# Kernel optimization log

Measured on AMD Instinct MI355X. Metric: run time of the kernel, lower is better.

Reference implementation:

```python
import jax, jax.numpy as jnp
import numpy as np

B, L, D = 8, 1024, 1024  # L must equal D for the elementwise sqrt(K) divide to broadcast


def setup_inputs() -> dict:
    key = jax.random.key(0)
    ks = jax.random.split(key, 9)
    # Non-negative inputs/weights/biases so K = x @ Wk.T + bk >= 0 and sqrt(K) is finite.
    rc = jax.random.uniform(ks[0], (B, L, D), dtype=jnp.float32)
    ri = jax.random.uniform(ks[1], (B, L, D), dtype=jnp.float32)
    tc = jax.random.uniform(ks[2], (B, L, D), dtype=jnp.float32)
    scale = 0.02
    Wq = jax.random.uniform(ks[3], (D, D), dtype=jnp.float32) * scale
    Wk = jax.random.uniform(ks[4], (D, D), dtype=jnp.float32) * scale
    Wv = jax.random.uniform(ks[5], (D, D), dtype=jnp.float32) * scale
    bq = jax.random.uniform(ks[6], (D,), dtype=jnp.float32) * scale
    bk = jax.random.uniform(ks[7], (D,), dtype=jnp.float32) * scale
    bv = jax.random.uniform(ks[8], (D,), dtype=jnp.float32) * scale
    return {
        "reference_caption": rc,
        "reference_image": ri,
        "target_caption": tc,
        "Wq": Wq, "bq": bq,
        "Wk": Wk, "bk": bk,
        "Wv": Wv, "bv": bv,
    }


def reference(reference_caption, reference_image, target_caption, Wq, bq, Wk, bk, Wv, bv):
    # torch nn.Linear: y = x @ W.T + b
    Q = reference_caption @ Wq.T + bq          # [B, Lq, D]
    K = reference_image @ Wk.T + bk            # [B, Lk, D]
    V = reference_image @ Wv.T + bv            # [B, Lk, D]
    matmul_qk = jnp.einsum("bqd,bkd->bqk", Q, K)  # [B, Lq, Lk]
    # Faithful to source: elementwise divide by sqrt(K) tensor (broadcasts since Lq==Lk==D).
    scaled_logits = matmul_qk / jnp.sqrt(K)
    attention_weights = jax.nn.softmax(scaled_logits, axis=-1)
    output = jnp.einsum("bqk,bkd->bqd", attention_weights, V)
    return (output, attention_weights)
```

## Files before the change

kernel.cpp:

```cpp
#include <hip/hip_runtime.h>
#include <hip/hip_fp16.h>
#include <math.h>

typedef unsigned short u16;
typedef __attribute__((ext_vector_type(8))) _Float16 half8;
typedef __attribute__((ext_vector_type(4))) float f32x4;

#define ASLOT 4096
#define SLOT  12288

__device__ __forceinline__ u16 f2h(float f){ __half h=__float2half(f); u16 r; __builtin_memcpy(&r,&h,2); return r; }
__device__ __forceinline__ float h2f(u16 u){ __half h; __builtin_memcpy(&h,&u,2); return __half2float(h); }

template<int ROWS>
__device__ __forceinline__ void stage_tile(const u16* __restrict__ G, int rowbase, int ldg,
                                           int k0, u16* Ls, int tid){
#pragma unroll
    for (int p = 0; p < ROWS / 64; ++p){
        const int lin = tid + p * 256;
        const int row = lin >> 2;
        const int cg  = ((lin & 3) ^ ((row >> 1) & 3)) * 8;
        const u16* g = G + (size_t)(rowbase + row) * ldg + (k0 + cg);
        __builtin_amdgcn_global_load_lds(
            (__attribute__((address_space(1))) void*)g,
            (__attribute__((address_space(3))) void*)(Ls + (size_t)lin * 8), 16, 0, 0);
    }
}

template<int EPI, int BIASM>
__device__ __forceinline__ void gemm_core(
    const u16* __restrict__ A, const u16* __restrict__ B,
    const float* __restrict__ bias,
    float* __restrict__ of, u16* __restrict__ oh,
    const float* __restrict__ cm, u16* __restrict__ od,
    int by, int bx, int lda, int ldb, int ldc, int K, u16* sh)
{
    const int tid  = threadIdx.x;
    const int lane = tid & 63, wv = tid >> 6;
    const int wr = (wv >> 1) * 64;
    const int wc = (wv & 1) * 128;
    const int row0 = by * 128, col0 = bx * 256;
    const int lr = lane & 15, hi = lane >> 4;
    const int co = (hi ^ ((lr >> 1) & 3)) * 8;

    f32x4 acc[4][8];
#pragma unroll
    for (int m = 0; m < 4; m++)
#pragma unroll
        for (int n = 0; n < 8; n++) acc[m][n] = (f32x4){0.f, 0.f, 0.f, 0.f};

    auto stage_set = [&](int buf, int k0){
        u16* s = sh + buf * SLOT;
        stage_tile<128>(A, row0, lda, k0, s, tid);
        stage_tile<256>(B, col0, ldb, k0, s + ASLOT, tid);
    };

    const int NIT = K >> 5;
    stage_set(0, 0);
    stage_set(1, 32);
    int bufs = 2, bufr = 0;
    for (int t = 0; t < NIT; ++t){
        if (t + 2 < NIT){ stage_set(bufs, (t + 2) << 5); bufs = (bufs + 1 == 3) ? 0 : bufs + 1; }
        const int rem = NIT - 1 - t;
        if (rem >= 2)      asm volatile("s_waitcnt vmcnt(12)" ::: "memory");
        else if (rem == 1) asm volatile("s_waitcnt vmcnt(6)" ::: "memory");
        else               asm volatile("s_waitcnt vmcnt(0)" ::: "memory");
        __builtin_amdgcn_s_barrier();
        __builtin_amdgcn_sched_barrier(0);

        const u16* s = sh + bufr * SLOT;
        bufr = (bufr + 1 == 3) ? 0 : bufr + 1;

        half8 a[4], b[8];
#pragma unroll
        for (int m = 0; m < 4; m++) a[m] = *(const half8*)&s[(wr + m * 16 + lr) * 32 + co];
#pragma unroll
        for (int n = 0; n < 8; n++) b[n] = *(const half8*)&s[ASLOT + (wc + n * 16 + lr) * 32 + co];
#pragma unroll
        for (int m = 0; m < 4; m++)
#pragma unroll
            for (int n = 0; n < 8; n++)
                acc[m][n] = __builtin_amdgcn_mfma_f32_16x16x32_f16(a[m], b[n], acc[m][n], 0, 0, 0);
        __builtin_amdgcn_sched_barrier(0);
        __builtin_amdgcn_s_barrier();
    }

#pragma unroll
    for (int m = 0; m < 4; m++) {
        const int rb = row0 + wr + m * 16 + hi * 4;
#pragma unroll
        for (int n = 0; n < 8; n++) {
            const int c = col0 + wc + n * 16 + lr;
            const float bc = (BIASM == 1) ? bias[c] : 0.f;
#pragma unroll
            for (int q = 0; q < 4; q++) {
                const int r = rb + q;
                float v = acc[m][n][q] + bc;
                if (BIASM == 2) v += bias[r];
                const size_t idx = (size_t)r * ldc + c;
                if (EPI == 0) of[idx] = v;
                else if (EPI == 1) oh[idx] = f2h(v);
                else {
                    const float d  = v - cm[(size_t)((r >> 10) << 10) + c];
                    const u16  dh = f2h(d);
                    oh[idx] = dh;
                    od[idx] = f2h(d - h2f(dh));
                }
            }
        }
    }
}

__global__ __launch_bounds__(256, 2) void lin_qk_k(
    const u16* __restrict__ rc_h, const u16* __restrict__ ri_h,
    const u16* __restrict__ Wq_h, const u16* __restrict__ Wk_h,
    const float* __restrict__ bq, const float* __restrict__ bk,
    const float* __restrict__ cm,
    u16* __restrict__ Q_h, u16* __restrict__ Kd, u16* __restrict__ Krs)
{
    __shared__ __align__(16) u16 sh[3 * SLOT];
    const int nwg = gridDim.x, chunk = nwg >> 3;
    const int swz = ((int)blockIdx.x & 7) * chunk + ((int)blockIdx.x >> 3);
    const int p = swz & 1, t = swz >> 1;
    if (p == 0) {
        gemm_core<1, 1>(rc_h, Wq_h, bq, nullptr, Q_h, nullptr, nullptr,
                        t >> 2, t & 3, 1024, 1024, 1024, 1024, sh);
    } else {
        gemm_core<5, 1>(ri_h, Wk_h, bk, nullptr, Kd, cm, Krs,
                        t >> 2, t & 3, 1024, 1024, 1024, 1024, sh);
    }
}

__global__ __launch_bounds__(256, 2) void qkt_vt_k(
    const u16* __restrict__ Q_h, const u16* __restrict__ Kd,
    const u16* __restrict__ ri_h, const u16* __restrict__ Wv_h,
    const float* __restrict__ bv, const float* __restrict__ u,
    float* __restrict__ wts, u16* __restrict__ Vt)
{
    __shared__ __align__(16) u16 sh[3 * SLOT];
    const int nwg = gridDim.x, chunk = nwg >> 3;
    const int swz = ((int)blockIdx.x & 7) * chunk + ((int)blockIdx.x >> 3);
    const int p = swz & 1, t = swz >> 1;
    if (p == 0) {
        const int z = t >> 5, rem = t & 31;
        gemm_core<0, 2>(Q_h + ((size_t)z << 20), Kd + ((size_t)z << 20),
                        u + ((size_t)z << 10), wts + ((size_t)z << 20), nullptr,
                        nullptr, nullptr,
                        rem >> 2, rem & 3, 1024, 1024, 1024, 1024, sh);
    } else {
        gemm_core<1, 2>(Wv_h, ri_h, bv, nullptr, Vt, nullptr, nullptr,
                        t >> 5, t & 31, 1024, 1024, 8192, 1024, sh);
    }
}

__global__ __launch_bounds__(256, 2) void av_k(
    const u16* __restrict__ W_h, const u16* __restrict__ Vt, float* __restrict__ outp)
{
    __shared__ __align__(16) u16 sh[3 * SLOT];
    const int nwg = gridDim.x, chunk = nwg >> 3;
    const int wg = ((int)blockIdx.x & 7) * chunk + ((int)blockIdx.x >> 3);
    const int z = wg >> 5, rem = wg & 31;
    gemm_core<0, 0>(W_h + ((size_t)z << 20), Vt + (size_t)z * 1024,
                    nullptr, outp + ((size_t)z << 20), nullptr, nullptr, nullptr,
                    rem >> 2, rem & 3, 1024, 8192, 1024, 1024, sh);
}

__global__ __launch_bounds__(256)
void colmean_k(const u16* __restrict__ ri_h, float* __restrict__ xbar)
{
    const int b = blockIdx.x >> 5, sub = blockIdx.x & 31;
    const int dg = sub & 3, rg = sub >> 2;
    const int d = dg * 256 + threadIdx.x;
    const u16* base = ri_h + ((size_t)b << 20) + ((size_t)(rg * 128) << 10) + d;
    float s = 0.f;
#pragma unroll 4
    for (int r = 0; r < 128; ++r) s += h2f(base[(size_t)r << 10]);
    atomicAdd(&xbar[(b << 10) + d], s * (1.f / 1024.f));
}

template<bool BIAS, bool AFULL>
__global__ __launch_bounds__(256)
void rowdot_k(const u16* __restrict__ A, const float* __restrict__ B,
              const float* __restrict__ bias, float* __restrict__ out)
{
    const int o = blockIdx.x * 4 + (threadIdx.x >> 6);
    const int lane = threadIdx.x & 63;
    const int ar = AFULL ? o : (o & 1023);
    const int br = o >> 10;
    const u16* ap = A + ((size_t)ar << 10);
    const float* bp = B + ((size_t)br << 10);
    float s = 0.f;
#pragma unroll
    for (int j = 0; j < 16; ++j){ const int i = lane + (j << 6); s += h2f(ap[i]) * bp[i]; }
#pragma unroll
    for (int off = 32; off >= 1; off >>= 1) s += __shfl_xor(s, off);
    if (lane == 0) out[o] = s + (BIAS ? bias[ar] : 0.f);
}

__global__ __launch_bounds__(256)
void softmax_scale_k(float* __restrict__ W, const u16* __restrict__ Kd,
                     const u16* __restrict__ Krs, const float* __restrict__ cm,
                     u16* __restrict__ Wh)
{
    const long row = blockIdx.x;
    const int b = (int)(row >> 10);
    float* p = W + (row << 10);
    const int tid = threadIdx.x;

    float4 v = ((const float4*)p)[tid];
    const ushort4 kd = ((const ushort4*)(Kd + (row << 10)))[tid];
    const ushort4 ks = ((const ushort4*)(Krs + (row << 10)))[tid];
    const float4 cmv = ((const float4*)(cm + ((size_t)b << 10)))[tid];
    v.x *= rsqrtf(h2f(kd.x) + h2f(ks.x) + cmv.x);
    v.y *= rsqrtf(h2f(kd.y) + h2f(ks.y) + cmv.y);
    v.z *= rsqrtf(h2f(kd.z) + h2f(ks.z) + cmv.z);
    v.w *= rsqrtf(h2f(kd.w) + h2f(ks.w) + cmv.w);

    float m = fmaxf(fmaxf(v.x, v.y), fmaxf(v.z, v.w));
#pragma unroll
    for (int o = 32; o >= 1; o >>= 1) m = fmaxf(m, __shfl_xor(m, o));
    __shared__ float sm[4];
    const int wid = tid >> 6, lane = tid & 63;
    if (lane == 0) sm[wid] = m;
    __syncthreads();
    m = fmaxf(fmaxf(sm[0], sm[1]), fmaxf(sm[2], sm[3]));

    v.x = __expf(v.x - m); v.y = __expf(v.y - m);
    v.z = __expf(v.z - m); v.w = __expf(v.w - m);
    float s = v.x + v.y + v.z + v.w;
#pragma unroll
    for (int o = 32; o >= 1; o >>= 1) s += __shfl_xor(s, o);
    __shared__ float ss[4];
    if (lane == 0) ss[wid] = s;
    __syncthreads();
    s = ss[0] + ss[1] + ss[2] + ss[3];

    const float inv = 1.0f / s;
    v.x *= inv; v.y *= inv; v.z *= inv; v.w *= inv;
    ((float4*)p)[tid] = v;

    ushort4 ub;
    ub.x = f2h(v.x); ub.y = f2h(v.y); ub.z = f2h(v.z); ub.w = f2h(v.w);
    ((ushort4*)(Wh + (row << 10)))[tid] = ub;
}

__global__ __launch_bounds__(256)
void conv_plain5_k(const float4* __restrict__ x0, ushort4* __restrict__ y0,
                   const float4* __restrict__ x1, ushort4* __restrict__ y1,
                   const float4* __restrict__ x2, ushort4* __restrict__ y2,
                   const float4* __restrict__ x3, ushort4* __restrict__ y3,
                   const float4* __restrict__ x4, ushort4* __restrict__ y4)
{
    const long i = (long)blockIdx.x * 256 + threadIdx.x;
    const long n0 = 2097152, n1 = 262144;
    const float4* x; ushort4* y; long j;
    if (i < n0)                 { x = x0; y = y0; j = i; }
    else if (i < 2*n0)          { x = x1; y = y1; j = i - n0; }
    else if (i < 2*n0 + n1)     { x = x2; y = y2; j = i - 2*n0; }
    else if (i < 2*n0 + 2*n1)   { x = x3; y = y3; j = i - 2*n0 - n1; }
    else                        { x = x4; y = y4; j = i - 2*n0 - 2*n1; }
    const float4 v = x[j];
    ushort4 o;
    o.x = f2h(v.x); o.y = f2h(v.y); o.z = f2h(v.z); o.w = f2h(v.w);
    y[j] = o;
}

extern "C" void kernel_launch(void* const* d_in, const int* in_sizes, int n_in,
                              void* d_out, int out_size, void* d_ws, size_t ws_size,
                              hipStream_t stream)
{
    const float* rc = (const float*)d_in[0];
    const float* ri = (const float*)d_in[1];
    const float* Wq = (const float*)d_in[3];
    const float* bq = (const float*)d_in[4];
    const float* Wk = (const float*)d_in[5];
    const float* bk = (const float*)d_in[6];
    const float* Wv = (const float*)d_in[7];
    const float* bv = (const float*)d_in[8];

    const long M8 = 8192 * 1024L;
    const long M1 = 1024 * 1024L;

    u16* ws   = (u16*)d_ws;
    u16* ri_h = ws;
    u16* rc_h = ws + 1 * M8;
    u16* Kd   = ws + 2 * M8;
    u16* Krs  = ws + 3 * M8;
    u16* Wq_h = ws + 4 * M8;
    u16* Wk_h = Wq_h + M1;
    u16* Wv_h = Wk_h + M1;
    float* xbar = (float*)(ws + 4 * M8 + 3 * M1);
    float* cm   = xbar + 8192;
    float* uu   = cm + 8192;

    float* outp = (float*)d_out;
    float* wts  = outp + M8;
    u16*   Q_h  = (u16*)d_out;
    u16*   Vt   = rc_h;
    u16*   W_h  = ri_h;

    conv_plain5_k<<<19456, 256, 0, stream>>>(
        (const float4*)ri, (ushort4*)ri_h, (const float4*)rc, (ushort4*)rc_h,
        (const float4*)Wq, (ushort4*)Wq_h, (const float4*)Wk, (ushort4*)Wk_h,
        (const float4*)Wv, (ushort4*)Wv_h);

    hipMemsetAsync(xbar, 0, 8192 * sizeof(float), stream);
    colmean_k<<<256, 256, 0, stream>>>(ri_h, xbar);

    rowdot_k<true, false><<<2048, 256, 0, stream>>>(Wk_h, xbar, bk, cm);

    lin_qk_k<<<512, 256, 0, stream>>>(rc_h, ri_h, Wq_h, Wk_h, bq, bk, cm, Q_h, Kd, Krs);

    rowdot_k<false, true><<<2048, 256, 0, stream>>>(Q_h, cm, nullptr, uu);

    qkt_vt_k<<<512, 256, 0, stream>>>(Q_h, Kd, ri_h, Wv_h, bv, uu, wts, Vt);

    softmax_scale_k<<<8192, 256, 0, stream>>>(wts, Kd, Krs, cm, W_h);

    av_k<<<256, 256, 0, stream>>>(W_h, Vt, outp);
}
```

Measured before the change: 166.4 us.

## Use 256x256 tiles with 8-wave ping-pong pipelined GEMM for projection kernels

Replaces the 128x256, 4-wave, triple-buffered GEMM core with a 256x256-tile, 512-thread, double-buffered core for the Q/K projection and QK^T/V^T kernels. The new core uses K-steps of 64, an 8-column XOR swizzle, and interleaves staging loads with MFMA phases using barriers and s_setprio. The aim is higher arithmetic intensity per tile and better overlap of loads with MFMA. In exchange it launches half as many workgroups at one block per CU, which could leave CUs underused, and it needs 128KB of LDS. The AV kernel keeps the old core under a new name.

```diff
diff --git a/kernel.cpp b/kernel.cpp
--- a/kernel.cpp
+++ b/kernel.cpp
@@ -12,23 +12,14 @@
 __device__ __forceinline__ u16 f2h(float f){ __half h=__float2half(f); u16 r; __builtin_memcpy(&r,&h,2); return r; }
 __device__ __forceinline__ float h2f(u16 u){ __half h; __builtin_memcpy(&h,&u,2); return __half2float(h); }
 
-template<int ROWS>
-__device__ __forceinline__ void stage_tile(const u16* __restrict__ G, int rowbase, int ldg,
-                                           int k0, u16* Ls, int tid){
-#pragma unroll
-    for (int p = 0; p < ROWS / 64; ++p){
-        const int lin = tid + p * 256;
-        const int row = lin >> 2;
-        const int cg  = ((lin & 3) ^ ((row >> 1) & 3)) * 8;
-        const u16* g = G + (size_t)(rowbase + row) * ldg + (k0 + cg);
-        __builtin_amdgcn_global_load_lds(
-            (__attribute__((address_space(1))) void*)g,
-            (__attribute__((address_space(3))) void*)(Ls + (size_t)lin * 8), 16, 0, 0);
-    }
-}
+#define SYNC1 do{ __builtin_amdgcn_sched_barrier(0); __builtin_amdgcn_s_barrier(); \
+    asm volatile("s_waitcnt lgkmcnt(0)" ::: "memory"); __builtin_amdgcn_sched_barrier(0); \
+    __builtin_amdgcn_s_setprio(1); }while(0)
+#define SYNC2 do{ __builtin_amdgcn_s_setprio(0); __builtin_amdgcn_sched_barrier(0); \
+    __builtin_amdgcn_s_barrier(); }while(0)
 
 template<int EPI, int BIASM>
-__device__ __forceinline__ void gemm_core(
+__device__ __forceinline__ void gemm8(
     const u16* __restrict__ A, const u16* __restrict__ B,
     const float* __restrict__ bias,
     float* __restrict__ of, u16* __restrict__ oh,
@@ -37,63 +28,111 @@
 {
     const int tid  = threadIdx.x;
     const int lane = tid & 63, wv = tid >> 6;
-    const int wr = (wv >> 1) * 64;
-    const int wc = (wv & 1) * 128;
-    const int row0 = by * 128, col0 = bx * 256;
+    const int wr = (wv >> 2) * 128;
+    const int wc = (wv & 3) * 64;
+    const int row0 = by * 256, col0 = bx * 256;
     const int lr = lane & 15, hi = lane >> 4;
-    const int co = (hi ^ ((lr >> 1) & 3)) * 8;
-
-    f32x4 acc[4][8];
-#pragma unroll
-    for (int m = 0; m < 4; m++)
-#pragma unroll
-        for (int n = 0; n < 8; n++) acc[m][n] = (f32x4){0.f, 0.f, 0.f, 0.f};
-
-    auto stage_set = [&](int buf, int k0){
-        u16* s = sh + buf * SLOT;
-        stage_tile<128>(A, row0, lda, k0, s, tid);
-        stage_tile<256>(B, col0, ldb, k0, s + ASLOT, tid);
+
+    f32x4 acc[8][4];
+#pragma unroll
+    for (int m = 0; m < 8; m++)
+#pragma unroll
+        for (int n = 0; n < 4; n++) acc[m][n] = (f32x4){0.f, 0.f, 0.f, 0.f};
+
+    auto STG = [&](int op, int kt, int half){
+        const u16* G = op ? B : A;
+        const int  ld = op ? ldb : lda;
+        const int  rb = (op ? col0 : row0) + half * 128;
+        const int  k0 = kt << 6;
+        u16* dst = sh + ((kt & 1) << 15) + (op << 14) + (half << 13);
+#pragma unroll
+        for (int p = 0; p < 2; ++p){
+            const int lin = tid + p * 512;
+            const int r   = lin >> 3;
+            const int cg  = (lin & 7) ^ (r & 7);
+            const u16* g = G + (size_t)(rb + r) * ld + k0 + cg * 8;
+            __builtin_amdgcn_global_load_lds(
+                (__attribute__((address_space(1))) void*)g,
+                (__attribute__((address_space(3))) void*)(dst + (size_t)lin * 8), 16, 0, 0);
+        }
     };
-
-    const int NIT = K >> 5;
-    stage_set(0, 0);
-    stage_set(1, 32);
-    int bufs = 2, bufr = 0;
-    for (int t = 0; t < NIT; ++t){
-        if (t + 2 < NIT){ stage_set(bufs, (t + 2) << 5); bufs = (bufs + 1 == 3) ? 0 : bufs + 1; }
-        const int rem = NIT - 1 - t;
-        if (rem >= 2)      asm volatile("s_waitcnt vmcnt(12)" ::: "memory");
-        else if (rem == 1) asm volatile("s_waitcnt vmcnt(6)" ::: "memory");
-        else               asm volatile("s_waitcnt vmcnt(0)" ::: "memory");
-        __builtin_amdgcn_s_barrier();
-        __builtin_amdgcn_sched_barrier(0);
-
-        const u16* s = sh + bufr * SLOT;
-        bufr = (bufr + 1 == 3) ? 0 : bufr + 1;
-
-        half8 a[4], b[8];
-#pragma unroll
-        for (int m = 0; m < 4; m++) a[m] = *(const half8*)&s[(wr + m * 16 + lr) * 32 + co];
-#pragma unroll
-        for (int n = 0; n < 8; n++) b[n] = *(const half8*)&s[ASLOT + (wc + n * 16 + lr) * 32 + co];
-#pragma unroll
-        for (int m = 0; m < 4; m++)
-#pragma unroll
-            for (int n = 0; n < 8; n++)
-                acc[m][n] = __builtin_amdgcn_mfma_f32_16x16x32_f16(a[m], b[n], acc[m][n], 0, 0, 0);
-        __builtin_amdgcn_sched_barrier(0);
-        __builtin_amdgcn_s_barrier();
-    }
-
-#pragma unroll
-    for (int m = 0; m < 4; m++) {
+    auto LDA_ = [&](half8* a, int kt, int mh){
+        const u16* base = sh + ((kt & 1) << 15) + ((wr >> 7) << 13);
+#pragma unroll
+        for (int mi = 0; mi < 4; ++mi)
+#pragma unroll
+            for (int ks = 0; ks < 2; ++ks){
+                const int row = (mh * 4 + mi) * 16 + lr;
+                a[mi * 2 + ks] = *(const half8*)&base[row * 64 + (((hi + ks * 4) ^ (lr & 7)) * 8)];
+            }
+    };
+    auto LDB_ = [&](half8* b, int kt, int nh){
+        const u16* base = sh + ((kt & 1) << 15) + 16384 + ((wc >> 7) << 13);
+        const int wcl = wc & 127;
+#pragma unroll
+        for (int ni = 0; ni < 2; ++ni)
+#pragma unroll
+            for (int ks = 0; ks < 2; ++ks){
+                const int row = wcl + (nh * 2 + ni) * 16 + lr;
+                b[ni * 2 + ks] = *(const half8*)&base[row * 64 + (((hi + ks * 4) ^ (lr & 7)) * 8)];
+            }
+    };
+    auto MM = [&](half8* a, half8* b, int mh, int nh){
+#pragma unroll
+        for (int mi = 0; mi < 4; ++mi)
+#pragma unroll
+            for (int ni = 0; ni < 2; ++ni)
+#pragma unroll
+                for (int ks = 0; ks < 2; ++ks)
+                    acc[mh * 4 + mi][nh * 2 + ni] = __builtin_amdgcn_mfma_f32_16x16x32_f16(
+                        a[mi * 2 + ks], b[ni * 2 + ks], acc[mh * 4 + mi][nh * 2 + ni], 0, 0, 0);
+    };
+
+    const int NKT = K >> 6, NIT = NKT >> 1;
+    STG(0, 0, 0); STG(0, 0, 1); STG(1, 0, 0); STG(1, 0, 1);
+    STG(1, 1, 0); STG(1, 1, 1); STG(0, 1, 0);
+    asm volatile("s_waitcnt vmcnt(6)" ::: "memory");
+    __builtin_amdgcn_s_barrier();
+
+    half8 a[8], b0[4], b1[4];
+    for (int i = 0; i < NIT; ++i){
+        const int t0 = 2 * i, t1 = 2 * i + 1;
+        const bool m0 = (t0 + 2 < NKT), m1 = (t1 + 2 < NKT);
+        LDA_(a, t0, 0); LDB_(b0, t0, 0);
+        STG(0, t1, 1);
+        SYNC1; MM(a, b0, 0, 0); SYNC2;
+        LDB_(b1, t0, 1);
+        SYNC1; MM(a, b1, 0, 1); SYNC2;
+        LDA_(a, t0, 1);
+        if (m0) STG(1, t0 + 2, 0);
+        SYNC1; MM(a, b1, 1, 1); SYNC2;
+        if (m0) { STG(1, t0 + 2, 1); STG(0, t0 + 2, 0); }
+        if (m0) asm volatile("s_waitcnt vmcnt(6)" ::: "memory");
+        else    asm volatile("s_waitcnt vmcnt(0)" ::: "memory");
+        SYNC1; MM(a, b0, 1, 0); SYNC2;
+        LDA_(a, t1, 0); LDB_(b0, t1, 0);
+        if (m0) STG(0, t0 + 2, 1);
+        SYNC1; MM(a, b0, 0, 0); SYNC2;
+        LDB_(b1, t1, 1);
+        SYNC1; MM(a, b1, 0, 1); SYNC2;
+        LDA_(a, t1, 1);
+        if (m1) STG(1, t1 + 2, 0);
+        SYNC1; MM(a, b1, 1, 1); SYNC2;
+        if (m1) { STG(1, t1 + 2, 1); STG(0, t1 + 2, 0); }
+        if (m1) asm volatile("s_waitcnt vmcnt(6)" ::: "memory");
+        else    asm volatile("s_waitcnt vmcnt(0)" ::: "memory");
+        SYNC1; MM(a, b0, 1, 0); SYNC2;
+    }
+
+#pragma unroll
+    for (int m = 0; m < 8; m++){
         const int rb = row0 + wr + m * 16 + hi * 4;
 #pragma unroll
-        for (int n = 0; n < 8; n++) {
+        for (int n = 0; n < 4; n++){
             const int c = col0 + wc + n * 16 + lr;
             const float bc = (BIASM == 1) ? bias[c] : 0.f;
 #pragma unroll
-            for (int q = 0; q < 4; q++) {
+            for (int q = 0; q < 4; q++){
                 const int r = rb + q;
                 float v = acc[m][n][q] + bc;
                 if (BIASM == 2) v += bias[r];
@@ -111,45 +150,126 @@
     }
 }
 
-__global__ __launch_bounds__(256, 2) void lin_qk_k(
+__global__ __launch_bounds__(512, 1) void lin_qk_k(
     const u16* __restrict__ rc_h, const u16* __restrict__ ri_h,
     const u16* __restrict__ Wq_h, const u16* __restrict__ Wk_h,
     const float* __restrict__ bq, const float* __restrict__ bk,
     const float* __restrict__ cm,
     u16* __restrict__ Q_h, u16* __restrict__ Kd, u16* __restrict__ Krs)
 {
-    __shared__ __align__(16) u16 sh[3 * SLOT];
+    __shared__ __align__(16) u16 sh[65536];
     const int nwg = gridDim.x, chunk = nwg >> 3;
     const int swz = ((int)blockIdx.x & 7) * chunk + ((int)blockIdx.x >> 3);
     const int p = swz & 1, t = swz >> 1;
     if (p == 0) {
-        gemm_core<1, 1>(rc_h, Wq_h, bq, nullptr, Q_h, nullptr, nullptr,
-                        t >> 2, t & 3, 1024, 1024, 1024, 1024, sh);
+        gemm8<1, 1>(rc_h, Wq_h, bq, nullptr, Q_h, nullptr, nullptr,
+                    t >> 2, t & 3, 1024, 1024, 1024, 1024, sh);
     } else {
-        gemm_core<5, 1>(ri_h, Wk_h, bk, nullptr, Kd, cm, Krs,
-                        t >> 2, t & 3, 1024, 1024, 1024, 1024, sh);
-    }
-}
-
-__global__ __launch_bounds__(256, 2) void qkt_vt_k(
+        gemm8<5, 1>(ri_h, Wk_h, bk, nullptr, Kd, cm, Krs,
+                    t >> 2, t & 3, 1024, 1024, 1024, 1024, sh);
+    }
+}
+
+__global__ __launch_bounds__(512, 1) void qkt_vt_k(
     const u16* __restrict__ Q_h, const u16* __restrict__ Kd,
     const u16* __restrict__ ri_h, const u16* __restrict__ Wv_h,
     const float* __restrict__ bv, const float* __restrict__ u,
     float* __restrict__ wts, u16* __restrict__ Vt)
 {
-    __shared__ __align__(16) u16 sh[3 * SLOT];
+    __shared__ __align__(16) u16 sh[65536];
     const int nwg = gridDim.x, chunk = nwg >> 3;
     const int swz = ((int)blockIdx.x & 7) * chunk + ((int)blockIdx.x >> 3);
     const int p = swz & 1, t = swz >> 1;
     if (p == 0) {
-        const int z = t >> 5, rem = t & 31;
-        gemm_core<0, 2>(Q_h + ((size_t)z << 20), Kd + ((size_t)z << 20),
-                        u + ((size_t)z << 10), wts + ((size_t)z << 20), nullptr,
-                        nullptr, nullptr,
-                        rem >> 2, rem & 3, 1024, 1024, 1024, 1024, sh);
+        const int z = t >> 4, rem = t & 15;
+        gemm8<0, 2>(Q_h + ((size_t)z << 20), Kd + ((size_t)z << 20),
+                    u + ((size_t)z << 10), wts + ((size_t)z << 20), nullptr,
+                    nullptr, nullptr,
+                    rem >> 2, rem & 3, 1024, 1024, 1024, 1024, sh);
     } else {
-        gemm_core<1, 2>(Wv_h, ri_h, bv, nullptr, Vt, nullptr, nullptr,
-                        t >> 5, t & 31, 1024, 1024, 8192, 1024, sh);
+        gemm8<1, 2>(Wv_h, ri_h, bv, nullptr, Vt, nullptr, nullptr,
+                    t >> 5, t & 31, 1024, 1024, 8192, 1024, sh);
+    }
+}
+
+__device__ __forceinline__ void stage_tile2(const u16* __restrict__ G, int rowbase, int ldg,
+                                            int k0, u16* Ls, int tid, int rows){
+    for (int p = 0; p < rows / 64; ++p){
+        const int lin = tid + p * 256;
+        const int row = lin >> 2;
+        const int cg  = ((lin & 3) ^ ((row >> 1) & 3)) * 8;
+        const u16* g = G + (size_t)(rowbase + row) * ldg + (k0 + cg);
+        __builtin_amdgcn_global_load_lds(
+            (__attribute__((address_space(1))) void*)g,
+            (__attribute__((address_space(3))) void*)(Ls + (size_t)lin * 8), 16, 0, 0);
+    }
+}
+
+__device__ __forceinline__ void gemm_core2(
+    const u16* __restrict__ A, const u16* __restrict__ B,
+    float* __restrict__ of,
+    int by, int bx, int lda, int ldb, int ldc, int K, u16* sh)
+{
+    const int tid  = threadIdx.x;
+    const int lane = tid & 63, wv = tid >> 6;
+    const int wr = (wv >> 1) * 64;
+    const int wc = (wv & 1) * 128;
+    const int row0 = by * 128, col0 = bx * 256;
+    const int lr = lane & 15, hi = lane >> 4;
+    const int co = (hi ^ ((lr >> 1) & 3)) * 8;
+
+    f32x4 acc[4][8];
+#pragma unroll
+    for (int m = 0; m < 4; m++)
+#pragma unroll
+        for (int n = 0; n < 8; n++) acc[m][n] = (f32x4){0.f, 0.f, 0.f, 0.f};
+
+    auto stage_set = [&](int buf, int k0){
+        u16* s = sh + buf * SLOT;
+        stage_tile2(A, row0, lda, k0, s, tid, 128);
+        stage_tile2(B, col0, ldb, k0, s + ASLOT, tid, 256);
+    };
+
+    const int NIT = K >> 5;
+    stage_set(0, 0);
+    stage_set(1, 32);
+    int bufs = 2, bufr = 0;
+    for (int t = 0; t < NIT; ++t){
+        if (t + 2 < NIT){ stage_set(bufs, (t + 2) << 5); bufs = (bufs + 1 == 3) ? 0 : bufs + 1; }
+        const int rem = NIT - 1 - t;
+        if (rem >= 2)      asm volatile("s_waitcnt vmcnt(12)" ::: "memory");
+        else if (rem == 1) asm volatile("s_waitcnt vmcnt(6)" ::: "memory");
+        else               asm volatile("s_waitcnt vmcnt(0)" ::: "memory");
+        __builtin_amdgcn_s_barrier();
+        __builtin_amdgcn_sched_barrier(0);
+
+        const u16* s = sh + bufr * SLOT;
+        bufr = (bufr + 1 == 3) ? 0 : bufr + 1;
+
+        half8 a[4], b[8];
+#pragma unroll
+        for (int m = 0; m < 4; m++) a[m] = *(const half8*)&s[(wr + m * 16 + lr) * 32 + co];
+#pragma unroll
+        for (int n = 0; n < 8; n++) b[n] = *(const half8*)&s[ASLOT + (wc + n * 16 + lr) * 32 + co];
+#pragma unroll
+        for (int m = 0; m < 4; m++)
+#pragma unroll
+            for (int n = 0; n < 8; n++)
+                acc[m][n] = __builtin_amdgcn_mfma_f32_16x16x32_f16(a[m], b[n], acc[m][n], 0, 0, 0);
+        __builtin_amdgcn_sched_barrier(0);
+        __builtin_amdgcn_s_barrier();
+    }
+
+#pragma unroll
+    for (int m = 0; m < 4; m++) {
+        const int rb = row0 + wr + m * 16 + hi * 4;
+#pragma unroll
+        for (int n = 0; n < 8; n++) {
+            const int c = col0 + wc + n * 16 + lr;
+#pragma unroll
+            for (int q = 0; q < 4; q++)
+                of[(size_t)(rb + q) * ldc + c] = acc[m][n][q];
+        }
     }
 }
 
@@ -160,9 +280,9 @@
     const int nwg = gridDim.x, chunk = nwg >> 3;
     const int wg = ((int)blockIdx.x & 7) * chunk + ((int)blockIdx.x >> 3);
     const int z = wg >> 5, rem = wg & 31;
-    gemm_core<0, 0>(W_h + ((size_t)z << 20), Vt + (size_t)z * 1024,
-                    nullptr, outp + ((size_t)z << 20), nullptr, nullptr, nullptr,
-                    rem >> 2, rem & 3, 1024, 8192, 1024, 1024, sh);
+    gemm_core2(W_h + ((size_t)z << 20), Vt + (size_t)z * 1024,
+               outp + ((size_t)z << 20),
+               rem >> 2, rem & 3, 1024, 8192, 1024, 1024, sh);
 }
 
 __global__ __launch_bounds__(256)
@@ -306,14 +426,13 @@
 
     hipMemsetAsync(xbar, 0, 8192 * sizeof(float), stream);
     colmean_k<<<256, 256, 0, stream>>>(ri_h, xbar);
-
     rowdot_k<true, false><<<2048, 256, 0, stream>>>(Wk_h, xbar, bk, cm);
 
-    lin_qk_k<<<512, 256, 0, stream>>>(rc_h, ri_h, Wq_h, Wk_h, bq, bk, cm, Q_h, Kd, Krs);
+    lin_qk_k<<<256, 512, 0, stream>>>(rc_h, ri_h, Wq_h, Wk_h, bq, bk, cm, Q_h, Kd, Krs);
 
     rowdot_k<false, true><<<2048, 256, 0, stream>>>(Q_h, cm, nullptr, uu);
 
-    qkt_vt_k<<<512, 256, 0, stream>>>(Q_h, Kd, ri_h, Wv_h, bv, uu, wts, Vt);
+    qkt_vt_k<<<256, 512, 0, stream>>>(Q_h, Kd, ri_h, Wv_h, bv, uu, wts, Vt);
 
     softmax_scale_k<<<8192, 256, 0, stream>>>(wts, Kd, Krs, cm, W_h);
 
```

Result: faster. 158.4 us (-4.8%).
